# Kernel tuning notes

Hardware: AMD Instinct MI355X
Metric: run time of the kernel (lower is better)

## Reference

```python
import jax, jax.numpy as jnp
import numpy as np

DIM = 384
HEADS = 6
K = 3  # kernel_size, stride = 1


def setup_inputs() -> dict:
    key = jax.random.key(0)
    ks = jax.random.split(key, 7)
    B, H, W, C = 16, 56, 56, DIM
    sc = 1.0 / np.sqrt(C)
    return {
        "x_map": jax.random.normal(ks[0], (B, H, W, C), dtype=jnp.float32),
        # Linear weights stored [in, out] (torch stores [out, in]; math identical)
        "W_attn": jax.random.normal(ks[1], (C, HEADS * K * K), dtype=jnp.float32) * sc,
        "b_attn": jax.random.normal(ks[2], (HEADS * K * K,), dtype=jnp.float32) * 0.02,
        "W_v": jax.random.normal(ks[3], (C, C), dtype=jnp.float32) * sc,
        "b_v": jax.random.normal(ks[4], (C,), dtype=jnp.float32) * 0.02,
        "W_proj": jax.random.normal(ks[5], (C, C), dtype=jnp.float32) * sc,
        "b_proj": jax.random.normal(ks[6], (C,), dtype=jnp.float32) * 0.02,
    }


def reference(x_map, W_attn, b_attn, W_v, b_v, W_proj, b_proj):
    B, H, W, C = x_map.shape
    k, heads = K, HEADS
    hd = C // heads
    pad = k // 2

    # attention logits per output pixel: [B, H*W, heads, k*k], softmax over window
    a = x_map @ W_attn + b_attn                     # [B,H,W,heads*k*k]
    a = jax.nn.softmax(a.reshape(B, H * W, heads, k * k), axis=-1)

    v = x_map @ W_v + b_v                           # [B,H,W,C]
    vp = jnp.pad(v, ((0, 0), (pad, pad), (pad, pad), (0, 0)))
    # k*k shifted views == F.unfold with row-major (ki,kj) kernel order
    patches = jnp.stack(
        [vp[:, i:i + H, j:j + W, :] for i in range(k) for j in range(k)],
        axis=3,
    )                                               # [B,H,W,k*k,C]
    patches = patches.reshape(B, H * W, k * k, heads, hd)

    # softmax-weighted sum over the k*k window, per head
    y = jnp.einsum('bpKhd,bphK->bphd', patches, a)  # [B,H*W,heads,hd]
    y = y.reshape(B, H, W, C)
    return y @ W_proj + b_proj
```

## Files before the change

### kernel.cpp

```cpp
#include <hip/hip_runtime.h>
#include <math.h>

#define NPIX 50176
#define CDIM 384
#define HEADS 6
#define NLOGIT 54
#define HH 56
#define WW 56
#define NCAT 448
#define KSTEPS 12
#define NCH_V 28
#define NCH_P 24

typedef __attribute__((ext_vector_type(8))) __bf16 bf16x8;
typedef __attribute__((ext_vector_type(4))) float f32x4;

__device__ __forceinline__ void glds16(const void* g, void* l) {
  __builtin_amdgcn_global_load_lds(
      (const __attribute__((address_space(1))) unsigned int*)g,
      (__attribute__((address_space(3))) unsigned int*)l, 16, 0, 0);
}

__global__ __launch_bounds__(256) void prep_kernel(
    const float* __restrict__ W_v, const float* __restrict__ W_proj,
    const float* __restrict__ W_attn, const float* __restrict__ b_attn,
    __bf16* __restrict__ Wcat_frag, __bf16* __restrict__ Wtp_frag,
    float* __restrict__ bpad) {
  const int gid = blockIdx.x * 256 + threadIdx.x;
  const int NV = KSTEPS * NCH_V * 64;
  const int NP = KSTEPS * NCH_P * 64;
  if (gid < NV) {
    const int ks   = gid / (NCH_V * 64);
    const int rem  = gid % (NCH_V * 64);
    const int ni   = rem >> 6;
    const int lane = rem & 63;
    const int n  = ni * 16 + (lane & 15);
    const int kb = ks * 32 + (lane >> 4) * 8;
    bf16x8 o;
    #pragma unroll
    for (int q = 0; q < 8; ++q) {
      const int k = kb + q;
      float val;
      if (n < CDIM) val = W_v[k * CDIM + n];
      else {
        const int nn = n - CDIM;
        val = (nn < NLOGIT) ? W_attn[k * NLOGIT + nn] : 0.f;
      }
      o[q] = (__bf16)val;
    }
    *(bf16x8*)&Wcat_frag[(size_t)gid * 8] = o;
  } else if (gid < NV + NP) {
    const int r    = gid - NV;
    const int ks   = r / (NCH_P * 64);
    const int rem  = r % (NCH_P * 64);
    const int ni   = rem >> 6;
    const int lane = rem & 63;
    const int n  = ni * 16 + (lane & 15);
    const int kb = ks * 32 + (lane >> 4) * 8;
    bf16x8 o;
    #pragma unroll
    for (int q = 0; q < 8; ++q) o[q] = (__bf16)W_proj[(kb + q) * CDIM + n];
    *(bf16x8*)&Wtp_frag[(size_t)r * 8] = o;
  } else if (gid < NV + NP + 64) {
    const int n = gid - NV - NP;
    bpad[n] = (n < NLOGIT) ? b_attn[n] : 0.f;
  }
}

__global__ __launch_bounds__(256) void gemm_v_logit_kernel(
    const float* __restrict__ X, const __bf16* __restrict__ Wcat_frag,
    const float* __restrict__ b_v, __bf16* __restrict__ v,
    const float* __restrict__ bpad, float* __restrict__ attn) {
  __shared__ char smem[2 * 14 * 1024];
  float (*Ls)[68] = (float(*)[68])smem;

  const int tid  = threadIdx.x;
  const int wave = tid >> 6;
  const int lane = tid & 63;
  const int bm   = blockIdx.x * 64;
  const int by   = blockIdx.y;
  const int nbase = by * 14;
  const int frow = lane & 15;
  const int fk8  = (lane >> 4) * 8;

  const int arow = bm + wave * 16 + frow;
  const float* xrow = X + (size_t)arow * CDIM + fk8;

  f32x4 acc[14] = {};

  #pragma unroll
  for (int c = 0; c < 4; ++c) {
    const int chunk = wave * 4 + c;
    if (chunk < 14)
      glds16(Wcat_frag + ((size_t)(0 * NCH_V + nbase + chunk) * 64 + lane) * 8,
             (__bf16*)smem + chunk * 512);
  }
  float4 pa0 = *(const float4*)(xrow + 0);
  float4 pa1 = *(const float4*)(xrow + 4);
  __syncthreads();

  int buf = 0;
  for (int ks = 0; ks < KSTEPS; ++ks) {
    if (ks + 1 < KSTEPS) {
      __bf16* dst = (__bf16*)smem + (buf ^ 1) * 14 * 512;
      #pragma unroll
      for (int c = 0; c < 4; ++c) {
        const int chunk = wave * 4 + c;
        if (chunk < 14)
          glds16(Wcat_frag +
                     ((size_t)((ks + 1) * NCH_V + nbase + chunk) * 64 + lane) * 8,
                 dst + chunk * 512);
      }
    }
    bf16x8 a;
    a[0] = (__bf16)pa0.x; a[1] = (__bf16)pa0.y; a[2] = (__bf16)pa0.z; a[3] = (__bf16)pa0.w;
    a[4] = (__bf16)pa1.x; a[5] = (__bf16)pa1.y; a[6] = (__bf16)pa1.z; a[7] = (__bf16)pa1.w;
    if (ks + 1 < KSTEPS) {
      pa0 = *(const float4*)(xrow + (ks + 1) * 32 + 0);
      pa1 = *(const float4*)(xrow + (ks + 1) * 32 + 4);
    }

    const __bf16* Bc = (const __bf16*)smem + buf * 14 * 512;
    #pragma unroll
    for (int ni = 0; ni < 14; ++ni) {
      const bf16x8 b = *(const bf16x8*)&Bc[(ni * 64 + lane) * 8];
      acc[ni] = __builtin_amdgcn_mfma_f32_16x16x32_bf16(a, b, acc[ni], 0, 0, 0);
    }
    __syncthreads();
    buf ^= 1;
  }

  const int orow = (lane >> 4) * 4;
  const int nv = (by == 0) ? 14 : 10;

  #pragma unroll
  for (int ni = 0; ni < 14; ++ni) {
    if (ni < nv) {
      const int n = by * 224 + ni * 16 + frow;
      const float bvl = b_v[n];
      #pragma unroll
      for (int r = 0; r < 4; ++r) {
        const int m = bm + wave * 16 + orow + r;
        v[(size_t)m * CDIM + n] = (__bf16)(acc[ni][r] + bvl);
      }
    }
  }

  if (by == 1) {
    float bvl[4];
    #pragma unroll
    for (int ni = 0; ni < 4; ++ni) bvl[ni] = bpad[ni * 16 + frow];
    #pragma unroll
    for (int ni = 0; ni < 4; ++ni)
      #pragma unroll
      for (int r = 0; r < 4; ++r)
        Ls[wave * 16 + orow + r][ni * 16 + frow] = acc[10 + ni][r] + bvl[ni];
    __syncthreads();

    #pragma unroll
    for (int it = 0; it < 2; ++it) {
      const int task = it * 256 + tid;
      if (task < 64 * HEADS) {
        const int pl = task / HEADS;
        const int h  = task % HEADS;
        const float* row = &Ls[pl][h * 9];
        float m = row[0];
        #pragma unroll
        for (int w = 1; w < 9; ++w) m = fmaxf(m, row[w]);
        float e[9], s = 0.f;
        #pragma unroll
        for (int w = 0; w < 9; ++w) { e[w] = __expf(row[w] - m); s += e[w]; }
        const float inv = 1.f / s;
        float* op = &attn[(size_t)(bm + pl) * NLOGIT + h * 9];
        #pragma unroll
        for (int w = 0; w < 9; ++w) op[w] = e[w] * inv;
      }
    }
  }
}

__global__ __launch_bounds__(256) void gemm_proj_kernel(
    const __bf16* __restrict__ Y, const __bf16* __restrict__ Wtp_frag,
    const float* __restrict__ bias, float* __restrict__ Out) {
  __shared__ __bf16 Bs[2 * 12 * 512];

  const int tid  = threadIdx.x;
  const int wave = tid >> 6;
  const int lane = tid & 63;
  const int bm   = blockIdx.x * 64;
  const int by   = blockIdx.y;
  const int nbase = by * 12;
  const int frow = lane & 15;
  const int fk8  = (lane >> 4) * 8;

  const int arow = bm + wave * 16 + frow;
  const __bf16* yrow = Y + (size_t)arow * CDIM + fk8;

  f32x4 acc[12] = {};

  #pragma unroll
  for (int c = 0; c < 3; ++c) {
    const int chunk = wave * 3 + c;
    glds16(Wtp_frag + ((size_t)(nbase + chunk) * 64 + lane) * 8,
           Bs + chunk * 512);
  }
  bf16x8 a = *(const bf16x8*)(yrow);
  __syncthreads();

  int buf = 0;
  for (int ks = 0; ks < KSTEPS; ++ks) {
    if (ks + 1 < KSTEPS) {
      __bf16* dst = Bs + (buf ^ 1) * 12 * 512;
      #pragma unroll
      for (int c = 0; c < 3; ++c) {
        const int chunk = wave * 3 + c;
        glds16(Wtp_frag +
                   ((size_t)((ks + 1) * NCH_P + nbase + chunk) * 64 + lane) * 8,
               dst + chunk * 512);
      }
    }
    bf16x8 a_next;
    if (ks + 1 < KSTEPS) a_next = *(const bf16x8*)(yrow + (ks + 1) * 32);

    const __bf16* Bc = Bs + buf * 12 * 512;
    #pragma unroll
    for (int ni = 0; ni < 12; ++ni) {
      const bf16x8 b = *(const bf16x8*)&Bc[(ni * 64 + lane) * 8];
      acc[ni] = __builtin_amdgcn_mfma_f32_16x16x32_bf16(a, b, acc[ni], 0, 0, 0);
    }
    __syncthreads();
    buf ^= 1;
    a = a_next;
  }

  const int orow = (lane >> 4) * 4;
  #pragma unroll
  for (int ni = 0; ni < 12; ++ni) {
    const int n = by * 192 + ni * 16 + frow;
    const float bvl = bias[n];
    #pragma unroll
    for (int r = 0; r < 4; ++r) {
      const int m = bm + wave * 16 + orow + r;
      Out[(size_t)m * CDIM + n] = acc[ni][r] + bvl;
    }
  }
}

__global__ __launch_bounds__(256) void aggregate_kernel(
    const __bf16* __restrict__ v, const float* __restrict__ attn,
    __bf16* __restrict__ y) {
  const int idx = blockIdx.x * 256 + threadIdx.x;
  const int cg = idx % 48;
  const int pg = idx / 48;
  const int c  = cg * 8;
  const int b  = pg / ((HH / 4) * WW);
  const int r2 = pg % ((HH / 4) * WW);
  const int i0 = (r2 / WW) * 4;
  const int j  = r2 % WW;
  const int head = c >> 6;

  const int pbase = (b * HH + i0) * WW + j;
  float aw[4][9];
  #pragma unroll
  for (int p = 0; p < 4; ++p) {
    const float* ap = attn + (size_t)(pbase + p * WW) * NLOGIT + head * 9;
    #pragma unroll
    for (int w = 0; w < 9; ++w) aw[p][w] = ap[w];
  }

  const bool j0ok = (j > 0), j2ok = (j < WW - 1);
  float acc[4][8] = {};

  #pragma unroll
  for (int li = 0; li < 6; ++li) {
    const int ii = i0 - 1 + li;
    if (ii < 0 || ii >= HH) continue;
    const __bf16* vrow = v + ((size_t)(b * HH + ii) * WW + j) * CDIM + c;
    float ch[3][8];
    #pragma unroll
    for (int kj = 0; kj < 3; ++kj) {
      const bool ok = (kj == 0) ? j0ok : (kj == 2) ? j2ok : true;
      if (ok) {
        const bf16x8 vv = *(const bf16x8*)(vrow + (kj - 1) * CDIM);
        #pragma unroll
        for (int q = 0; q < 8; ++q) ch[kj][q] = (float)vv[q];
      } else {
        #pragma unroll
        for (int q = 0; q < 8; ++q) ch[kj][q] = 0.f;
      }
    }
    #pragma unroll
    for (int p = 0; p < 4; ++p) {
      const int ki = li - p;
      if (ki < 0 || ki > 2) continue;
      #pragma unroll
      for (int kj = 0; kj < 3; ++kj) {
        const float w = aw[p][ki * 3 + kj];
        #pragma unroll
        for (int q = 0; q < 8; ++q) acc[p][q] += w * ch[kj][q];
      }
    }
  }

  #pragma unroll
  for (int p = 0; p < 4; ++p) {
    bf16x8 o;
    #pragma unroll
    for (int q = 0; q < 8; ++q) o[q] = (__bf16)acc[p][q];
    *(bf16x8*)&y[(size_t)(pbase + p * WW) * CDIM + c] = o;
  }
}

extern "C" void kernel_launch(void* const* d_in, const int* in_sizes, int n_in,
                              void* d_out, int out_size, void* d_ws,
                              size_t ws_size, hipStream_t stream) {
  const float* x      = (const float*)d_in[0];
  const float* W_attn = (const float*)d_in[1];
  const float* b_attn = (const float*)d_in[2];
  const float* W_v    = (const float*)d_in[3];
  const float* b_v    = (const float*)d_in[4];
  const float* W_proj = (const float*)d_in[5];
  const float* b_proj = (const float*)d_in[6];
  float* out = (float*)d_out;

  char* w = (char*)d_ws;
  __bf16* v    = (__bf16*)w;  w += (size_t)NPIX * CDIM * 2;
  __bf16* y    = (__bf16*)w;  w += (size_t)NPIX * CDIM * 2;
  float*  attn = (float*)w;   w += (size_t)NPIX * NLOGIT * 4;
  __bf16* Wcat_frag = (__bf16*)w;  w += (size_t)NCAT * CDIM * 2;
  __bf16* Wtp_frag  = (__bf16*)w;  w += (size_t)CDIM * CDIM * 2;
  float*  bpad = (float*)w;   w += 64 * 4;

  const int prep_n = KSTEPS * NCH_V * 64 + KSTEPS * NCH_P * 64 + 64;
  prep_kernel<<<(prep_n + 255) / 256, 256, 0, stream>>>(
      W_v, W_proj, W_attn, b_attn, Wcat_frag, Wtp_frag, bpad);

  gemm_v_logit_kernel<<<dim3(NPIX / 64, 2), 256, 0, stream>>>(
      x, Wcat_frag, b_v, v, bpad, attn);

  aggregate_kernel<<<(NPIX / 4 * 48) / 256, 256, 0, stream>>>(v, attn, y);

  gemm_proj_kernel<<<dim3(NPIX / 64, 2), 256, 0, stream>>>(
      y, Wtp_frag, b_proj, out);
}
```

Before: 109.0 us.

## Triple-buffer weight tiles with one barrier per k-step in both GEMMs

Both GEMM kernels move from double-buffered LDS weight staging with two syncs per k-step to a three-stage ring that prefetches two k-steps ahead. Each step now does a partial s_waitcnt vmcnt plus a single s_barrier, and the A-operand register loads are double-buffered to match. The goal is to hide global-to-LDS latency and cut barrier stalls. In exchange LDS use grows by half, which may lower occupancy, and correctness now depends on hand-counted vmcnt values matching the number of outstanding loads per wave (waves with fewer chunks issue fewer loads).

```diff
diff --git a/kernel.cpp b/kernel.cpp
--- a/kernel.cpp
+++ b/kernel.cpp
@@ -71,8 +71,8 @@
     const float* __restrict__ X, const __bf16* __restrict__ Wcat_frag,
     const float* __restrict__ b_v, __bf16* __restrict__ v,
     const float* __restrict__ bpad, float* __restrict__ attn) {
-  __shared__ char smem[2 * 14 * 1024];
-  float (*Ls)[68] = (float(*)[68])smem;
+  __shared__ __bf16 Bs[3 * 14 * 512];
+  float (*Ls)[68] = (float(*)[68])Bs;
 
   const int tid  = threadIdx.x;
   const int wave = tid >> 6;
@@ -87,47 +87,61 @@
   const float* xrow = X + (size_t)arow * CDIM + fk8;
 
   f32x4 acc[14] = {};
-
+  float4 pa[2][2];
+
+  pa[0][0] = *(const float4*)(xrow + 0);
+  pa[0][1] = *(const float4*)(xrow + 4);
   #pragma unroll
   for (int c = 0; c < 4; ++c) {
     const int chunk = wave * 4 + c;
     if (chunk < 14)
-      glds16(Wcat_frag + ((size_t)(0 * NCH_V + nbase + chunk) * 64 + lane) * 8,
-             (__bf16*)smem + chunk * 512);
-  }
-  float4 pa0 = *(const float4*)(xrow + 0);
-  float4 pa1 = *(const float4*)(xrow + 4);
-  __syncthreads();
-
-  int buf = 0;
+      glds16(Wcat_frag + ((size_t)(nbase + chunk) * 64 + lane) * 8,
+             Bs + chunk * 512);
+  }
+  pa[1][0] = *(const float4*)(xrow + 32);
+  pa[1][1] = *(const float4*)(xrow + 36);
+  #pragma unroll
+  for (int c = 0; c < 4; ++c) {
+    const int chunk = wave * 4 + c;
+    if (chunk < 14)
+      glds16(Wcat_frag + ((size_t)(NCH_V + nbase + chunk) * 64 + lane) * 8,
+             Bs + 14 * 512 + chunk * 512);
+  }
+
+  #pragma unroll
   for (int ks = 0; ks < KSTEPS; ++ks) {
-    if (ks + 1 < KSTEPS) {
-      __bf16* dst = (__bf16*)smem + (buf ^ 1) * 14 * 512;
+    if (ks < KSTEPS - 1) {
+      asm volatile("s_waitcnt vmcnt(6)" ::: "memory");
+    } else {
+      asm volatile("s_waitcnt vmcnt(0)" ::: "memory");
+    }
+    __builtin_amdgcn_s_barrier();
+
+    const float4 q0 = pa[ks & 1][0], q1 = pa[ks & 1][1];
+    bf16x8 a;
+    a[0] = (__bf16)q0.x; a[1] = (__bf16)q0.y; a[2] = (__bf16)q0.z; a[3] = (__bf16)q0.w;
+    a[4] = (__bf16)q1.x; a[5] = (__bf16)q1.y; a[6] = (__bf16)q1.z; a[7] = (__bf16)q1.w;
+
+    if (ks + 2 < KSTEPS) {
+      pa[ks & 1][0] = *(const float4*)(xrow + (ks + 2) * 32 + 0);
+      pa[ks & 1][1] = *(const float4*)(xrow + (ks + 2) * 32 + 4);
+      __bf16* dst = Bs + ((ks + 2) % 3) * 14 * 512;
       #pragma unroll
       for (int c = 0; c < 4; ++c) {
         const int chunk = wave * 4 + c;
         if (chunk < 14)
           glds16(Wcat_frag +
-                     ((size_t)((ks + 1) * NCH_V + nbase + chunk) * 64 + lane) * 8,
+                     ((size_t)((ks + 2) * NCH_V + nbase + chunk) * 64 + lane) * 8,
                  dst + chunk * 512);
       }
     }
-    bf16x8 a;
-    a[0] = (__bf16)pa0.x; a[1] = (__bf16)pa0.y; a[2] = (__bf16)pa0.z; a[3] = (__bf16)pa0.w;
-    a[4] = (__bf16)pa1.x; a[5] = (__bf16)pa1.y; a[6] = (__bf16)pa1.z; a[7] = (__bf16)pa1.w;
-    if (ks + 1 < KSTEPS) {
-      pa0 = *(const float4*)(xrow + (ks + 1) * 32 + 0);
-      pa1 = *(const float4*)(xrow + (ks + 1) * 32 + 4);
-    }
-
-    const __bf16* Bc = (const __bf16*)smem + buf * 14 * 512;
+
+    const __bf16* Bc = Bs + (ks % 3) * 14 * 512;
     #pragma unroll
     for (int ni = 0; ni < 14; ++ni) {
       const bf16x8 b = *(const bf16x8*)&Bc[(ni * 64 + lane) * 8];
       acc[ni] = __builtin_amdgcn_mfma_f32_16x16x32_bf16(a, b, acc[ni], 0, 0, 0);
     }
-    __syncthreads();
-    buf ^= 1;
   }
 
   const int orow = (lane >> 4) * 4;
@@ -147,6 +161,7 @@
   }
 
   if (by == 1) {
+    __syncthreads();
     float bvl[4];
     #pragma unroll
     for (int ni = 0; ni < 4; ++ni) bvl[ni] = bpad[ni * 16 + frow];
@@ -182,7 +197,7 @@
 __global__ __launch_bounds__(256) void gemm_proj_kernel(
     const __bf16* __restrict__ Y, const __bf16* __restrict__ Wtp_frag,
     const float* __restrict__ bias, float* __restrict__ Out) {
-  __shared__ __bf16 Bs[2 * 12 * 512];
+  __shared__ __bf16 Bs[3 * 12 * 512];
 
   const int tid  = threadIdx.x;
   const int wave = tid >> 6;
@@ -197,40 +212,52 @@
   const __bf16* yrow = Y + (size_t)arow * CDIM + fk8;
 
   f32x4 acc[12] = {};
-
+  bf16x8 pa[2];
+
+  pa[0] = *(const bf16x8*)(yrow + 0);
   #pragma unroll
   for (int c = 0; c < 3; ++c) {
     const int chunk = wave * 3 + c;
     glds16(Wtp_frag + ((size_t)(nbase + chunk) * 64 + lane) * 8,
            Bs + chunk * 512);
   }
-  bf16x8 a = *(const bf16x8*)(yrow);
-  __syncthreads();
-
-  int buf = 0;
+  pa[1] = *(const bf16x8*)(yrow + 32);
+  #pragma unroll
+  for (int c = 0; c < 3; ++c) {
+    const int chunk = wave * 3 + c;
+    glds16(Wtp_frag + ((size_t)(NCH_P + nbase + chunk) * 64 + lane) * 8,
+           Bs + 12 * 512 + chunk * 512);
+  }
+
+  #pragma unroll
   for (int ks = 0; ks < KSTEPS; ++ks) {
-    if (ks + 1 < KSTEPS) {
-      __bf16* dst = Bs + (buf ^ 1) * 12 * 512;
+    if (ks < KSTEPS - 1) {
+      asm volatile("s_waitcnt vmcnt(4)" ::: "memory");
+    } else {
+      asm volatile("s_waitcnt vmcnt(0)" ::: "memory");
+    }
+    __builtin_amdgcn_s_barrier();
+
+    const bf16x8 a = pa[ks & 1];
+
+    if (ks + 2 < KSTEPS) {
+      pa[ks & 1] = *(const bf16x8*)(yrow + (ks + 2) * 32);
+      __bf16* dst = Bs + ((ks + 2) % 3) * 12 * 512;
       #pragma unroll
       for (int c = 0; c < 3; ++c) {
         const int chunk = wave * 3 + c;
         glds16(Wtp_frag +
-                   ((size_t)((ks + 1) * NCH_P + nbase + chunk) * 64 + lane) * 8,
+                   ((size_t)((ks + 2) * NCH_P + nbase + chunk) * 64 + lane) * 8,
                dst + chunk * 512);
       }
     }
-    bf16x8 a_next;
-    if (ks + 1 < KSTEPS) a_next = *(const bf16x8*)(yrow + (ks + 1) * 32);
-
-    const __bf16* Bc = Bs + buf * 12 * 512;
+
+    const __bf16* Bc = Bs + (ks % 3) * 12 * 512;
     #pragma unroll
     for (int ni = 0; ni < 12; ++ni) {
       const bf16x8 b = *(const bf16x8*)&Bc[(ni * 64 + lane) * 8];
       acc[ni] = __builtin_amdgcn_mfma_f32_16x16x32_bf16(a, b, acc[ni], 0, 0, 0);
     }
-    __syncthreads();
-    buf ^= 1;
-    a = a_next;
   }
 
   const int orow = (lane >> 4) * 4;
```

Result: faster. 105.4 us (-3.3%).
